# Optimization experiments

Measured on AMD Instinct MI355X. Metric: run time of the kernel, lower is better.

Reference implementation:

```python
import jax, jax.numpy as jnp
import numpy as np

NEG = -9e15
ALPHA = 0.2  # leaky relu negative slope


def setup_inputs() -> dict:
    key = jax.random.key(0)
    k1, k2, k3, k4 = jax.random.split(key, 4)
    B, N, d = 8, 2048, 128
    h = jax.random.normal(k1, (B, N, d), dtype=jnp.float32)
    adj = jax.random.randint(k2, (B, N, N), 0, 2, dtype=jnp.int32)
    W = jax.random.normal(k3, (d, d), dtype=jnp.float32) * (1.414 / np.sqrt(d))
    a = jax.random.normal(k4, (2 * d, 1), dtype=jnp.float32) * 0.1
    return {"h": h, "adj": adj, "W": W, "a": a}


def reference(h, adj, W, a):
    d = W.shape[1]
    Wh = jnp.matmul(h, W)                       # [B, N, d]  (dropout p=0 -> identity)
    Wh1 = jnp.matmul(Wh, a[:d])                 # [B, N, 1]
    Wh2 = jnp.matmul(Wh, a[d:])                 # [B, N, 1]
    e = jax.nn.leaky_relu(Wh1 + jnp.swapaxes(Wh2, 1, 2), negative_slope=ALPHA)  # [B, N, N]
    scores = jnp.where(adj > 0, e, NEG)
    attention = jax.nn.softmax(scores, axis=-1)  # [B, N, N]
    h_prime = jnp.matmul(attention, Wh)          # [B, N, d]
    out = h + h_prime                            # residual=True, concat=False
    return out, attention
```

## Files before the change

kernel.cpp:

```cpp
#include <hip/hip_runtime.h>
#include <cstdint>
#include <cstddef>

typedef float  v4f __attribute__((ext_vector_type(4)));
typedef short  v8s __attribute__((ext_vector_type(8)));
typedef int    v4i __attribute__((ext_vector_type(4)));

#define BB 8
#define NN 2048
#define DD 128
#define TI 16
#define NEGV (-9e15f)

__device__ __forceinline__ unsigned short f2bf(float x) {
  unsigned u = __float_as_uint(x);
  u = u + 0x7FFFu + ((u >> 16) & 1u);
  return (unsigned short)(u >> 16);
}

__global__ __launch_bounds__(256) void gat_k1(
    const float* __restrict__ h, const float* __restrict__ W, const float* __restrict__ a,
    short* __restrict__ whbT, float* __restrict__ wh1g, float* __restrict__ wh2g)
{
  __shared__ __align__(16) unsigned short wT[DD * 136];
  __shared__ __align__(16) unsigned short staging[DD * 72];

  const int tid  = threadIdx.x;
  const int lane = tid & 63;
  const int wid  = tid >> 6;
  const int m16  = lane & 15;
  const int quad = lane >> 4;
  const int b    = blockIdx.y;
  const int i0   = blockIdx.x * 64;

  {
    const v4f* W4 = (const v4f*)W;
    #pragma unroll
    for (int it = 0; it < 16; it++) {
      int idx = it * 256 + tid;
      int k  = idx >> 5;
      int c4 = (idx & 31) * 4;
      v4f wv = W4[idx];
      #pragma unroll
      for (int q = 0; q < 4; q++)
        wT[(c4 + q) * 136 + k] = f2bf(wv[q]);
    }
  }

  const float* hrow = h + (size_t)(b * NN + i0 + wid * 16 + m16) * DD;
  v8s af[4];
  #pragma unroll
  for (int ks = 0; ks < 4; ks++) {
    v4f x0 = *(const v4f*)(hrow + ks * 32 + quad * 8);
    v4f x1 = *(const v4f*)(hrow + ks * 32 + quad * 8 + 4);
    v8s t;
    t[0] = (short)f2bf(x0.x); t[1] = (short)f2bf(x0.y);
    t[2] = (short)f2bf(x0.z); t[3] = (short)f2bf(x0.w);
    t[4] = (short)f2bf(x1.x); t[5] = (short)f2bf(x1.y);
    t[6] = (short)f2bf(x1.z); t[7] = (short)f2bf(x1.w);
    af[ks] = t;
  }
  __syncthreads();

  v4f acc[8];
  #pragma unroll
  for (int t = 0; t < 8; t++) acc[t] = (v4f){0.f, 0.f, 0.f, 0.f};

  #pragma unroll
  for (int ks = 0; ks < 4; ks++) {
    #pragma unroll
    for (int t = 0; t < 8; t++) {
      v8s bf = *(const v8s*)&wT[(t * 16 + m16) * 136 + ks * 32 + quad * 8];
      acc[t] = __builtin_amdgcn_mfma_f32_16x16x32_bf16(af[ks], bf, acc[t], 0, 0, 0);
    }
  }

  {
    float a1v[8], a2v[8];
    #pragma unroll
    for (int t = 0; t < 8; t++) {
      a1v[t] = a[t * 16 + m16];
      a2v[t] = a[DD + t * 16 + m16];
    }
    #pragma unroll
    for (int r = 0; r < 4; r++) {
      float p1 = 0.f, p2 = 0.f;
      #pragma unroll
      for (int t = 0; t < 8; t++) {
        p1 += acc[t][r] * a1v[t];
        p2 += acc[t][r] * a2v[t];
      }
      #pragma unroll
      for (int off = 8; off > 0; off >>= 1) {
        p1 += __shfl_xor(p1, off);
        p2 += __shfl_xor(p2, off);
      }
      if (m16 == 0) {
        int gi = b * NN + i0 + wid * 16 + quad * 4 + r;
        wh1g[gi] = p1;
        wh2g[gi] = p2;
      }
    }
  }

  #pragma unroll
  for (int t = 0; t < 8; t++)
    #pragma unroll
    for (int r = 0; r < 4; r++)
      staging[(t * 16 + m16) * 72 + wid * 16 + quad * 4 + r] = f2bf(acc[t][r]);
  __syncthreads();

  #pragma unroll
  for (int it = 0; it < 4; it++) {
    int idx = it * 256 + tid;
    int c  = idx >> 3;
    int i8 = idx & 7;
    v8s val = *(const v8s*)&staging[c * 72 + i8 * 8];
    *(v8s*)(whbT + (size_t)b * DD * NN + (size_t)c * NN + i0 + i8 * 8) = val;
  }
}

__global__ __launch_bounds__(256) void gat_k0(
    const int* __restrict__ adj, const float* __restrict__ wh1g,
    const float* __restrict__ wh2g, unsigned* __restrict__ maskg,
    float* __restrict__ msg, float* __restrict__ rsg)
{
  const int tid  = threadIdx.x;
  const int lane = tid & 63;
  const int wid  = tid >> 6;
  const int b    = blockIdx.y;
  const int i    = blockIdx.x * 4 + wid;
  const size_t row = (size_t)b * NN + i;

  const v4i* arow = (const v4i*)(adj + row * NN);
  const v4f* w2   = (const v4f*)(wh2g + (size_t)b * NN);
  const float wh1v = wh1g[row];

  float e[32];
  float m = -INFINITY;
  unsigned mbits = 0u;
  #pragma unroll
  for (int u = 0; u < 8; u++) {
    v4i av  = __builtin_nontemporal_load(&arow[u * 64 + lane]);
    v4f w2v = w2[u * 64 + lane];
    #pragma unroll
    for (int q = 0; q < 4; q++) {
      bool mk = av[q] > 0;
      float x = wh1v + w2v[q];
      float ev = mk ? (x > 0.f ? x : 0.2f * x) : NEGV;
      e[u * 4 + q] = ev;
      m = fmaxf(m, ev);
      mbits |= (mk ? 1u : 0u) << (u * 4 + q);
    }
  }
  maskg[row * 64 + lane] = mbits;

  #pragma unroll
  for (int off = 32; off > 0; off >>= 1) m = fmaxf(m, __shfl_xor(m, off));
  float s = 0.f;
  #pragma unroll
  for (int k = 0; k < 32; k++) s += __expf(e[k] - m);
  #pragma unroll
  for (int off = 32; off > 0; off >>= 1) s += __shfl_xor(s, off);

  if (lane == 0) { msg[row] = m; rsg[row] = 1.f / s; }
}

__global__ __launch_bounds__(256, 4) void gat_k2(
    const float* __restrict__ h, const unsigned* __restrict__ maskg,
    const short* __restrict__ whbT, const float* __restrict__ wh1g,
    const float* __restrict__ wh2g, const float* __restrict__ msg,
    const float* __restrict__ rsg, float* __restrict__ out,
    float* __restrict__ attout)
{
  __shared__ __align__(16) float smem[4 * TI * DD];
  __shared__ unsigned masks[TI * 68];
  __shared__ float wh1s[TI], ms_s[TI], rs_s[TI];

  const int tid  = threadIdx.x;
  const int lane = tid & 63;
  const int wid  = tid >> 6;
  const int m16  = lane & 15;
  const int quad = lane >> 4;
  const int b    = blockIdx.y;
  const int i0   = blockIdx.x * TI;

  float* wh2s = smem;
  {
    const v4f* w2g4 = (const v4f*)(wh2g + (size_t)b * NN);
    ((v4f*)wh2s)[tid]       = w2g4[tid];
    ((v4f*)wh2s)[tid + 256] = w2g4[tid + 256];
  }
  {
    const unsigned* mg = maskg + (size_t)(b * NN + i0) * 64;
    #pragma unroll
    for (int it = 0; it < 4; it++) {
      int idx = it * 256 + tid;
      masks[(idx >> 6) * 68 + (idx & 63)] = mg[idx];
    }
  }
  if (tid < TI) {
    wh1s[tid] = wh1g[b * NN + i0 + tid];
    ms_s[tid] = msg[b * NN + i0 + tid];
    rs_s[tid] = rsg[b * NN + i0 + tid];
  }
  __syncthreads();

  const float wh1v = wh1s[m16];
  const float mi   = ms_s[m16];
  const float rsi  = rs_s[m16];
  const short* whbT_b = whbT + (size_t)b * DD * NN;
  float* attrow = attout + (size_t)(b * NN + i0 + m16) * NN;

  v4f acc[8];
  #pragma unroll
  for (int t = 0; t < 8; t++) acc[t] = (v4f){0.f, 0.f, 0.f, 0.f};

  for (int c = 0; c < 8; c++) {
    const int j0   = wid * 512 + c * 64;
    const int ubit = (j0 >> 8) << 2;
    #pragma unroll
    for (int ks = 0; ks < 2; ks++) {
      const int jb = j0 + ks * 32 + quad * 8;
      v4f w2a = ((const v4f*)wh2s)[jb >> 2];
      v4f w2b = ((const v4f*)wh2s)[(jb >> 2) + 1];
      const int w0  = (jb >> 2) & 63;
      unsigned mwa = masks[m16 * 68 + w0];
      unsigned mwb = masks[m16 * 68 + w0 + 1];

      v4f at0, at1;
      v8s af;
      #pragma unroll
      for (int q = 0; q < 4; q++) {
        float x = wh1v + w2a[q];
        float ev = ((mwa >> (ubit + q)) & 1u) ? (x > 0.f ? x : 0.2f * x) : NEGV;
        float at = __expf(ev - mi) * rsi;
        at0[q] = at;
        af[q]  = (short)f2bf(at);
      }
      #pragma unroll
      for (int q = 0; q < 4; q++) {
        float x = wh1v + w2b[q];
        float ev = ((mwb >> (ubit + q)) & 1u) ? (x > 0.f ? x : 0.2f * x) : NEGV;
        float at = __expf(ev - mi) * rsi;
        at1[q] = at;
        af[4 + q] = (short)f2bf(at);
      }
      __builtin_nontemporal_store(at0, (v4f*)(attrow + jb));
      __builtin_nontemporal_store(at1, (v4f*)(attrow + jb + 4));

      #pragma unroll
      for (int t = 0; t < 8; t++) {
        v8s bf = *(const v8s*)(whbT_b + (size_t)(t * 16 + m16) * NN + jb);
        acc[t] = __builtin_amdgcn_mfma_f32_16x16x32_bf16(af, bf, acc[t], 0, 0, 0);
      }
    }
  }

  __syncthreads();
  float* red = smem;
  #pragma unroll
  for (int t = 0; t < 8; t++)
    #pragma unroll
    for (int r = 0; r < 4; r++)
      red[wid * (TI * DD) + (quad * 4 + r) * DD + t * 16 + m16] = acc[t][r];
  __syncthreads();

  {
    const size_t base = (size_t)(b * NN + i0) * DD;
    #pragma unroll
    for (int it = 0; it < 2; it++) {
      int idx = it * 256 + tid;
      v4f s0 = ((const v4f*)red)[idx];
      v4f s1 = ((const v4f*)red)[idx + 512];
      v4f s2 = ((const v4f*)red)[idx + 1024];
      v4f s3 = ((const v4f*)red)[idx + 1536];
      v4f hv = *(const v4f*)(h + base + (size_t)idx * 4);
      v4f o  = hv + s0 + s1 + s2 + s3;
      *(v4f*)(out + base + (size_t)idx * 4) = o;
    }
  }
}

extern "C" void kernel_launch(void* const* d_in, const int* in_sizes, int n_in,
                              void* d_out, int out_size, void* d_ws, size_t ws_size,
                              hipStream_t stream) {
  const float* h  = (const float*)d_in[0];
  const int* adj  = (const int*)d_in[1];
  const float* W  = (const float*)d_in[2];
  const float* a  = (const float*)d_in[3];

  float* out    = (float*)d_out;
  float* attout = out + (size_t)BB * NN * DD;

  char* ws = (char*)d_ws;
  short* whbT = (short*)ws;                      ws += (size_t)BB * DD * NN * 2;
  float* wh1  = (float*)ws;                      ws += (size_t)BB * NN * 4;
  float* wh2  = (float*)ws;                      ws += (size_t)BB * NN * 4;
  float* msg  = (float*)ws;                      ws += (size_t)BB * NN * 4;
  float* rsg  = (float*)ws;                      ws += (size_t)BB * NN * 4;
  unsigned* maskg = (unsigned*)ws;

  gat_k1<<<dim3(NN / 64, BB), 256, 0, stream>>>(h, W, a, whbT, wh1, wh2);
  gat_k0<<<dim3(NN / 4, BB), 256, 0, stream>>>(adj, wh1, wh2, maskg, msg, rsg);
  gat_k2<<<dim3(NN / TI, BB), 256, 0, stream>>>(h, maskg, whbT, wh1, wh2, msg, rsg, out, attout);
}
```

Before: 296.0 us.

## Double-buffer Wh B-fragment loads and use packed bf16 conversion in attention loop

Restructures the attention-times-Wh loop into 16 phases, each of which prefetches the next phase's B fragments into a second register buffer, with a sched_barrier, before it computes the current phase's softmax values and MFMAs. The aim is to hide global-load latency of whbT behind the exp and MFMA work. It also replaces the manual round-to-nearest bf16 packing with the hardware v_cvt_pk_bf16_f32 instruction, cutting ALU work. The extra buffer adds 32 VGPRs per thread, which could reduce occupancy. The last phase issues a wasted load that wraps around to the first chunk.

```diff
diff --git a/kernel.cpp b/kernel.cpp
--- a/kernel.cpp
+++ b/kernel.cpp
@@ -5,6 +5,7 @@
 typedef float  v4f __attribute__((ext_vector_type(4)));
 typedef short  v8s __attribute__((ext_vector_type(8)));
 typedef int    v4i __attribute__((ext_vector_type(4)));
+typedef unsigned int v4u __attribute__((ext_vector_type(4)));
 
 #define BB 8
 #define NN 2048
@@ -16,6 +17,12 @@
   unsigned u = __float_as_uint(x);
   u = u + 0x7FFFu + ((u >> 16) & 1u);
   return (unsigned short)(u >> 16);
+}
+
+__device__ __forceinline__ unsigned cvt_pk_bf16(float lo, float hi) {
+  unsigned r;
+  asm("v_cvt_pk_bf16_f32 %0, %1, %2" : "=v"(r) : "v"(lo), "v"(hi));
+  return r;
 }
 
 __global__ __launch_bounds__(256) void gat_k1(
@@ -216,45 +223,63 @@
   #pragma unroll
   for (int t = 0; t < 8; t++) acc[t] = (v4f){0.f, 0.f, 0.f, 0.f};
 
-  for (int c = 0; c < 8; c++) {
-    const int j0   = wid * 512 + c * 64;
-    const int ubit = (j0 >> 8) << 2;
-    #pragma unroll
-    for (int ks = 0; ks < 2; ks++) {
-      const int jb = j0 + ks * 32 + quad * 8;
-      v4f w2a = ((const v4f*)wh2s)[jb >> 2];
-      v4f w2b = ((const v4f*)wh2s)[(jb >> 2) + 1];
-      const int w0  = (jb >> 2) & 63;
-      unsigned mwa = masks[m16 * 68 + w0];
-      unsigned mwb = masks[m16 * 68 + w0 + 1];
-
-      v4f at0, at1;
-      v8s af;
-      #pragma unroll
-      for (int q = 0; q < 4; q++) {
-        float x = wh1v + w2a[q];
-        float ev = ((mwa >> (ubit + q)) & 1u) ? (x > 0.f ? x : 0.2f * x) : NEGV;
-        float at = __expf(ev - mi) * rsi;
-        at0[q] = at;
-        af[q]  = (short)f2bf(at);
-      }
-      #pragma unroll
-      for (int q = 0; q < 4; q++) {
-        float x = wh1v + w2b[q];
-        float ev = ((mwb >> (ubit + q)) & 1u) ? (x > 0.f ? x : 0.2f * x) : NEGV;
-        float at = __expf(ev - mi) * rsi;
-        at1[q] = at;
-        af[4 + q] = (short)f2bf(at);
-      }
-      __builtin_nontemporal_store(at0, (v4f*)(attrow + jb));
-      __builtin_nontemporal_store(at1, (v4f*)(attrow + jb + 4));
-
-      #pragma unroll
-      for (int t = 0; t < 8; t++) {
-        v8s bf = *(const v8s*)(whbT_b + (size_t)(t * 16 + m16) * NN + jb);
-        acc[t] = __builtin_amdgcn_mfma_f32_16x16x32_bf16(af, bf, acc[t], 0, 0, 0);
-      }
-    }
+  v8s bfr0[8], bfr1[8];
+
+  {
+    const int jb0 = wid * 512 + quad * 8;
+    #pragma unroll
+    for (int t = 0; t < 8; t++)
+      bfr0[t] = *(const v8s*)(whbT_b + (size_t)(t * 16 + m16) * NN + jb0);
+  }
+
+  auto phase = [&](int p, v8s (&cur)[8], v8s (&nxt)[8]) {
+    const int jb  = wid * 512 + ((p >> 1) << 6) + ((p & 1) << 5) + quad * 8;
+    const int pn  = (p + 1) & 15;
+    const int jbn = wid * 512 + ((pn >> 1) << 6) + ((pn & 1) << 5) + quad * 8;
+
+    #pragma unroll
+    for (int t = 0; t < 8; t++)
+      nxt[t] = *(const v8s*)(whbT_b + (size_t)(t * 16 + m16) * NN + jbn);
+    __builtin_amdgcn_sched_barrier(0);
+
+    const int ubit = (jb >> 8) << 2;
+    v4f w2a = ((const v4f*)wh2s)[jb >> 2];
+    v4f w2b = ((const v4f*)wh2s)[(jb >> 2) + 1];
+    const int w0 = (jb >> 2) & 63;
+    unsigned mwa = masks[m16 * 68 + w0];
+    unsigned mwb = masks[m16 * 68 + w0 + 1];
+
+    v4f at0, at1;
+    #pragma unroll
+    for (int q = 0; q < 4; q++) {
+      float x = wh1v + w2a[q];
+      float ev = ((mwa >> (ubit + q)) & 1u) ? (x > 0.f ? x : 0.2f * x) : NEGV;
+      at0[q] = __expf(ev - mi) * rsi;
+    }
+    #pragma unroll
+    for (int q = 0; q < 4; q++) {
+      float x = wh1v + w2b[q];
+      float ev = ((mwb >> (ubit + q)) & 1u) ? (x > 0.f ? x : 0.2f * x) : NEGV;
+      at1[q] = __expf(ev - mi) * rsi;
+    }
+    union { v4u u; v8s s; } af;
+    af.u[0] = cvt_pk_bf16(at0[0], at0[1]);
+    af.u[1] = cvt_pk_bf16(at0[2], at0[3]);
+    af.u[2] = cvt_pk_bf16(at1[0], at1[1]);
+    af.u[3] = cvt_pk_bf16(at1[2], at1[3]);
+
+    __builtin_nontemporal_store(at0, (v4f*)(attrow + jb));
+    __builtin_nontemporal_store(at1, (v4f*)(attrow + jb + 4));
+
+    #pragma unroll
+    for (int t = 0; t < 8; t++)
+      acc[t] = __builtin_amdgcn_mfma_f32_16x16x32_bf16(af.s, cur[t], acc[t], 0, 0, 0);
+  };
+
+  #pragma unroll 1
+  for (int pc = 0; pc < 8; pc++) {
+    phase(2 * pc,     bfr0, bfr1);
+    phase(2 * pc + 1, bfr1, bfr0);
   }
 
   __syncthreads();
```

After: 330.8 us. 11.7% more time.

## Coalesce attention stores via LDS transpose and prefetch B fragments in GAT kernel

Applied to the files above, without the earlier changes.

Reorganizes gat_k2 so each lane computes four consecutive attention values for one row. Each quad of 16 lanes now writes a contiguous 256-byte row segment, replacing scattered per-row stores. The bf16 attention values are staged through a per-wave LDS tile and re-read in MFMA A-fragment layout. Both halves of the Wh^T B-fragments are loaded up front to hide latency, packed bf16 conversion uses the hardware v_cvt_pk_bf16_f32 instruction, and the grid is flattened with batch interleaved across consecutive blocks. In exchange it adds LDS traffic and register pressure, and it relies on wave-level ordering of the LDS tile writes and reads without an explicit barrier.

```diff
diff --git a/kernel.cpp b/kernel.cpp
--- a/kernel.cpp
+++ b/kernel.cpp
@@ -5,6 +5,7 @@
 typedef float  v4f __attribute__((ext_vector_type(4)));
 typedef short  v8s __attribute__((ext_vector_type(8)));
 typedef int    v4i __attribute__((ext_vector_type(4)));
+typedef unsigned long long u64;
 
 #define BB 8
 #define NN 2048
@@ -16,6 +17,12 @@
   unsigned u = __float_as_uint(x);
   u = u + 0x7FFFu + ((u >> 16) & 1u);
   return (unsigned short)(u >> 16);
+}
+
+__device__ __forceinline__ unsigned cvt_pk_bf16(float lo, float hi) {
+  unsigned r;
+  asm("v_cvt_pk_bf16_f32 %0, %1, %2" : "=v"(r) : "v"(lo), "v"(hi));
+  return r;
 }
 
 __global__ __launch_bounds__(256) void gat_k1(
@@ -182,10 +189,13 @@
   const int wid  = tid >> 6;
   const int m16  = lane & 15;
   const int quad = lane >> 4;
-  const int b    = blockIdx.y;
-  const int i0   = blockIdx.x * TI;
+  const int bid  = blockIdx.x;
+  const int b    = bid & 7;
+  const int i0   = (bid >> 3) * TI;
 
   float* wh2s = smem;
+  unsigned short* atile = (unsigned short*)(smem + 2048) + wid * (TI * 68);
+
   {
     const v4f* w2g4 = (const v4f*)(wh2g + (size_t)b * NN);
     ((v4f*)wh2s)[tid]       = w2g4[tid];
@@ -206,55 +216,66 @@
   }
   __syncthreads();
 
-  const float wh1v = wh1s[m16];
-  const float mi   = ms_s[m16];
-  const float rsi  = rs_s[m16];
+  float wh1r[4], mir[4], rsr[4];
+  #pragma unroll
+  for (int it = 0; it < 4; it++) {
+    wh1r[it] = wh1s[it * 4 + quad];
+    mir[it]  = ms_s[it * 4 + quad];
+    rsr[it]  = rs_s[it * 4 + quad];
+  }
+
   const short* whbT_b = whbT + (size_t)b * DD * NN;
-  float* attrow = attout + (size_t)(b * NN + i0 + m16) * NN;
+  float* attbase = attout + (size_t)(b * NN + i0) * NN;
 
   v4f acc[8];
   #pragma unroll
   for (int t = 0; t < 8; t++) acc[t] = (v4f){0.f, 0.f, 0.f, 0.f};
 
   for (int c = 0; c < 8; c++) {
-    const int j0   = wid * 512 + c * 64;
+    const int j0 = wid * 512 + c * 64;
+    const int jb = j0 + quad * 8;
+
+    v8s bfr0[8], bfr1[8];
+    #pragma unroll
+    for (int t = 0; t < 8; t++)
+      bfr0[t] = *(const v8s*)(whbT_b + (size_t)(t * 16 + m16) * NN + jb);
+    #pragma unroll
+    for (int t = 0; t < 8; t++)
+      bfr1[t] = *(const v8s*)(whbT_b + (size_t)(t * 16 + m16) * NN + jb + 32);
+
     const int ubit = (j0 >> 8) << 2;
-    #pragma unroll
-    for (int ks = 0; ks < 2; ks++) {
-      const int jb = j0 + ks * 32 + quad * 8;
-      v4f w2a = ((const v4f*)wh2s)[jb >> 2];
-      v4f w2b = ((const v4f*)wh2s)[(jb >> 2) + 1];
-      const int w0  = (jb >> 2) & 63;
-      unsigned mwa = masks[m16 * 68 + w0];
-      unsigned mwb = masks[m16 * 68 + w0 + 1];
-
-      v4f at0, at1;
-      v8s af;
+    const int wq   = ((j0 >> 2) & 63) + m16;
+    v4f w2v = ((const v4f*)wh2s)[(j0 >> 2) + m16];
+    #pragma unroll
+    for (int it = 0; it < 4; it++) {
+      const int row = it * 4 + quad;
+      unsigned mw = masks[row * 68 + wq];
+      v4f at;
       #pragma unroll
       for (int q = 0; q < 4; q++) {
-        float x = wh1v + w2a[q];
-        float ev = ((mwa >> (ubit + q)) & 1u) ? (x > 0.f ? x : 0.2f * x) : NEGV;
-        float at = __expf(ev - mi) * rsi;
-        at0[q] = at;
-        af[q]  = (short)f2bf(at);
+        float x = wh1r[it] + w2v[q];
+        float ev = ((mw >> (ubit + q)) & 1u) ? (x > 0.f ? x : 0.2f * x) : NEGV;
+        at[q] = __expf(ev - mir[it]) * rsr[it];
       }
-      #pragma unroll
-      for (int q = 0; q < 4; q++) {
-        float x = wh1v + w2b[q];
-        float ev = ((mwb >> (ubit + q)) & 1u) ? (x > 0.f ? x : 0.2f * x) : NEGV;
-        float at = __expf(ev - mi) * rsi;
-        at1[q] = at;
-        af[4 + q] = (short)f2bf(at);
-      }
-      __builtin_nontemporal_store(at0, (v4f*)(attrow + jb));
-      __builtin_nontemporal_store(at1, (v4f*)(attrow + jb + 4));
-
-      #pragma unroll
-      for (int t = 0; t < 8; t++) {
-        v8s bf = *(const v8s*)(whbT_b + (size_t)(t * 16 + m16) * NN + jb);
-        acc[t] = __builtin_amdgcn_mfma_f32_16x16x32_bf16(af, bf, acc[t], 0, 0, 0);
-      }
-    }
+      __builtin_nontemporal_store(at, (v4f*)(attbase + (size_t)row * NN + j0 + m16 * 4));
+      unsigned lo = cvt_pk_bf16(at[0], at[1]);
+      unsigned hi = cvt_pk_bf16(at[2], at[3]);
+      u64 dv = (u64)lo | ((u64)hi << 32);
+      *(u64*)&atile[row * 68 + m16 * 4] = dv;
+    }
+
+    union { v8s s; u64 d[2]; } af0, af1;
+    af0.d[0] = *(const u64*)&atile[m16 * 68 + quad * 8];
+    af0.d[1] = *(const u64*)&atile[m16 * 68 + quad * 8 + 4];
+    af1.d[0] = *(const u64*)&atile[m16 * 68 + 32 + quad * 8];
+    af1.d[1] = *(const u64*)&atile[m16 * 68 + 32 + quad * 8 + 4];
+
+    #pragma unroll
+    for (int t = 0; t < 8; t++)
+      acc[t] = __builtin_amdgcn_mfma_f32_16x16x32_bf16(af0.s, bfr0[t], acc[t], 0, 0, 0);
+    #pragma unroll
+    for (int t = 0; t < 8; t++)
+      acc[t] = __builtin_amdgcn_mfma_f32_16x16x32_bf16(af1.s, bfr1[t], acc[t], 0, 0, 0);
   }
 
   __syncthreads();
@@ -303,5 +324,5 @@
 
   gat_k1<<<dim3(NN / 64, BB), 256, 0, stream>>>(h, W, a, whbT, wh1, wh2);
   gat_k0<<<dim3(NN / 4, BB), 256, 0, stream>>>(adj, wh1, wh2, maskg, msg, rsg);
-  gat_k2<<<dim3(NN / TI, BB), 256, 0, stream>>>(h, maskg, whbT, wh1, wh2, msg, rsg, out, attout);
-}
+  gat_k2<<<dim3(NN / TI * BB), 256, 0, stream>>>(h, maskg, whbT, wh1, wh2, msg, rsg, out, attout);
+}
```

Result: no change. 295.9 us (-0.0%).
